# Performance work log

Hardware: AMD Instinct MI355X
Metric: run time of the kernel (lower is better)

The kernel has to match this reference:

```python
import jax, jax.numpy as jnp
import numpy as np

V, B, T, E, H = 16384, 64, 256, 128, 1024


def setup_inputs() -> dict:
    key = jax.random.key(0)
    ks = jax.random.split(key, 10)
    inp = {
        'input_data': jax.random.randint(ks[0], (B, T), 0, V, dtype=jnp.int32),
        'targets': jax.random.randint(ks[1], (B, T), 0, V, dtype=jnp.int32),
        'embedding': jax.random.normal(ks[2], (V, E), dtype=jnp.float32) * 0.02,
        # layer 1 GRU (input E, hidden H): gate kernel [E+H, 2H], candidate kernel [E+H, H]
        'W_g1': jax.random.normal(ks[3], (E + H, 2 * H), dtype=jnp.float32) * 0.05,
        'b_g1': jnp.ones((2 * H,), dtype=jnp.float32),  # TF GRUCell gate bias init = 1.0
        'W_c1': jax.random.normal(ks[4], (E + H, H), dtype=jnp.float32) * 0.05,
        'b_c1': jnp.zeros((H,), dtype=jnp.float32),
        # layer 2 GRU (input H, hidden H)
        'W_g2': jax.random.normal(ks[5], (2 * H, 2 * H), dtype=jnp.float32) * 0.05,
        'b_g2': jnp.ones((2 * H,), dtype=jnp.float32),
        'W_c2': jax.random.normal(ks[6], (2 * H, H), dtype=jnp.float32) * 0.05,
        'b_c2': jnp.zeros((H,), dtype=jnp.float32),
        'softmax_w': jax.random.normal(ks[7], (H, V), dtype=jnp.float32) * 1e-4,
        'softmax_b': jnp.zeros((V,), dtype=jnp.float32),
    }
    return inp


def _gru_step(h, x, W_g, b_g, W_c, b_c):
    # TF GRUCell: r,u = sigmoid([x,h] @ W_g + b_g); c = tanh([x, r*h] @ W_c + b_c)
    ru = jax.nn.sigmoid(jnp.concatenate([x, h], axis=-1) @ W_g + b_g)
    r, u = jnp.split(ru, 2, axis=-1)
    c = jnp.tanh(jnp.concatenate([x, r * h], axis=-1) @ W_c + b_c)
    return u * h + (1.0 - u) * c


def reference(input_data, targets, embedding, W_g1, b_g1, W_c1, b_c1,
              W_g2, b_g2, W_c2, b_c2, softmax_w, softmax_b):
    # inference path: is_training=False, so dropout wrappers are identity
    x = embedding[input_data]               # [B, T, E]
    xs = jnp.transpose(x, (1, 0, 2))        # [T, B, E] time-major for scan

    h0 = (jnp.zeros((B, H), x.dtype), jnp.zeros((B, H), x.dtype))

    def step(carry, x_t):
        h1, h2 = carry
        h1 = _gru_step(h1, x_t, W_g1, b_g1, W_c1, b_c1)
        h2 = _gru_step(h2, h1, W_g2, b_g2, W_c2, b_c2)
        return (h1, h2), h2

    _, ys = jax.lax.scan(step, h0, xs)      # ys: [T, B, H]
    out = jnp.transpose(ys, (1, 0, 2)).reshape(-1, H)  # [B*T, H] batch-major flatten

    logits = out @ softmax_w + softmax_b    # [B*T, V]
    logp = jax.nn.log_softmax(logits, axis=-1)
    flat_t = targets.reshape(-1)
    nll = -jnp.take_along_axis(logp, flat_t[:, None], axis=1)[:, 0]
    loss = jnp.mean(nll)
    return logits, loss
```

## Files before the change

kernel.cpp:

```cpp
#include <hip/hip_runtime.h>

typedef __bf16 bf16_t;
typedef __bf16 bf16x8 __attribute__((ext_vector_type(8)));
typedef float f32x4 __attribute__((ext_vector_type(4)));
typedef float f32x2 __attribute__((ext_vector_type(2)));
typedef unsigned u32x4 __attribute__((ext_vector_type(4)));

constexpr int kB = 64, kT = 256, kE = 128, kH = 1024, kV = 16384;
constexpr int kBT = kB * kT;

__device__ __forceinline__ void ld16_sc(const void* p, u32x4& d) {
    asm volatile("global_load_dwordx4 %0, %1, off sc0 sc1" : "=v"(d) : "v"(p));
}
__device__ __forceinline__ void ld8_sc(const void* p, f32x2& d) {
    asm volatile("global_load_dwordx2 %0, %1, off sc0 sc1" : "=v"(d) : "v"(p));
}
__device__ __forceinline__ void ld8_c(const void* p, f32x2& d) {
    asm volatile("global_load_dwordx2 %0, %1, off" : "=v"(d) : "v"(p));
}
__device__ __forceinline__ void st4_sc(void* p, unsigned v) {
    asm volatile("global_store_dword %0, %1, off sc0 sc1" :: "v"(p), "v"(v));
}
__device__ __forceinline__ void st8_sc(void* p, f32x2 v) {
    asm volatile("global_store_dwordx2 %0, %1, off sc0 sc1" :: "v"(p), "v"(v));
}
__device__ __forceinline__ unsigned ld_flag(const unsigned* p) {
    unsigned v;
    asm volatile("global_load_dword %0, %1, off sc0 sc1\n\ts_waitcnt vmcnt(0)"
                 : "=v"(v) : "v"(p) : "memory");
    return v;
}
#define WAITVM(n) asm volatile("s_waitcnt vmcnt(" #n ")" ::: "memory")

#define GL2LDS(gp, lp) __builtin_amdgcn_global_load_lds( \
    (const __attribute__((address_space(1))) void*)(gp), \
    (__attribute__((address_space(3))) void*)(lp), 16, 0, 0)

__device__ __forceinline__ unsigned pack_bf16(float a, float b) {
    union { unsigned u; __bf16 h[2]; } c;
    c.h[0] = (__bf16)a; c.h[1] = (__bf16)b;
    return c.u;
}
__device__ __forceinline__ f32x2 mk2(float a, float b) {
    f32x2 v; v[0] = a; v[1] = b; return v;
}

__global__ void zero_bytes(char* p, size_t n) {
    size_t stride = (size_t)gridDim.x * blockDim.x * 16;
    for (size_t i = ((size_t)blockIdx.x * blockDim.x + threadIdx.x) * 16; i < n; i += stride) {
        uint4 z; z.x = z.y = z.z = z.w = 0;
        *reinterpret_cast<uint4*>(p + i) = z;
    }
}

__global__ void transpose_to_bf16(const float* __restrict__ src, bf16_t* __restrict__ dst,
                                  int R, int C) {
    __shared__ float tile[32][33];
    int c0 = blockIdx.x * 32, r0 = blockIdx.y * 32;
    for (int rr = threadIdx.y; rr < 32; rr += 8)
        tile[rr][threadIdx.x] = src[(size_t)(r0 + rr) * C + c0 + threadIdx.x];
    __syncthreads();
    for (int rr = threadIdx.y; rr < 32; rr += 8)
        dst[(size_t)(c0 + rr) * R + r0 + threadIdx.x] = (bf16_t)tile[threadIdx.x][rr];
}

__global__ __launch_bounds__(256) void embed_gather(const int* __restrict__ ids,
                                                    const float* __restrict__ emb,
                                                    bf16_t* __restrict__ XB) {
    int base = blockIdx.x * 16;
    for (int idx = threadIdx.x; idx < 16 * kE; idx += 256) {
        int r = idx >> 7, k = idx & 127;
        int row = base + r;
        XB[(size_t)row * kE + k] = (bf16_t)emb[(size_t)ids[row] * kE + k];
    }
}

__global__ __launch_bounds__(256) void xpre_gemm(
    const bf16_t* __restrict__ XB, const bf16_t* __restrict__ WT,
    const float* __restrict__ bias, float* __restrict__ Cout, int N) {
    __shared__ __align__(16) char As[128 * 256];
    __shared__ __align__(16) char Bs[128 * 256];
    const int tid = threadIdx.x;
    const int w = tid >> 6, l = tid & 63, lr = l & 15, lk8 = (l >> 4) * 8;
    const int wr = w >> 1, wc = w & 1;
    const size_t row0 = (size_t)blockIdx.y * 128, col0 = (size_t)blockIdx.x * 128;
    for (int c = tid; c < 2048; c += 256) {
        int o = c * 16; int row = o >> 8; int kk = o & 255;
        int dst = (row << 8) + (kk ^ ((row & 7) << 4));
        *reinterpret_cast<bf16x8*>(As + dst) =
            *reinterpret_cast<const bf16x8*>(XB + (row0 + row) * kE + (kk >> 1));
        *reinterpret_cast<bf16x8*>(Bs + dst) =
            *reinterpret_cast<const bf16x8*>(WT + (col0 + row) * kE + (kk >> 1));
    }
    __syncthreads();
    f32x4 acc[4][4] = {};
    #pragma unroll
    for (int ks = 0; ks < 4; ++ks) {
        int kb = (ks * 32 + lk8) * 2;
        bf16x8 af[4], bfv[4];
        #pragma unroll
        for (int mf = 0; mf < 4; ++mf) {
            int r = wr * 64 + mf * 16 + lr;
            af[mf] = *reinterpret_cast<const bf16x8*>(As + (r << 8) + (kb ^ ((r & 7) << 4)));
        }
        #pragma unroll
        for (int nf = 0; nf < 4; ++nf) {
            int r = wc * 64 + nf * 16 + lr;
            bfv[nf] = *reinterpret_cast<const bf16x8*>(Bs + (r << 8) + (kb ^ ((r & 7) << 4)));
        }
        #pragma unroll
        for (int mf = 0; mf < 4; ++mf)
            #pragma unroll
            for (int nf = 0; nf < 4; ++nf)
                acc[mf][nf] = __builtin_amdgcn_mfma_f32_16x16x32_bf16(af[mf], bfv[nf], acc[mf][nf], 0, 0, 0);
    }
    #pragma unroll
    for (int mf = 0; mf < 4; ++mf) {
        size_t row = row0 + wr * 64 + mf * 16 + (l >> 4) * 4;
        #pragma unroll
        for (int nf = 0; nf < 4; ++nf) {
            size_t col = col0 + wc * 64 + nf * 16 + lr;
            float bvl = bias[col];
            #pragma unroll
            for (int i = 0; i < 4; ++i)
                Cout[(row + i) * (size_t)N + col] = acc[mf][nf][i] + bvl;
        }
    }
}

struct PP {
    const bf16_t *WG1HT, *WC1HT, *WG2T, *WC2T;
    const float *XG1, *XC1;
    const float *bg2, *bc2;
    float *H1F, *H2F, *U1, *U2;
    bf16_t *X2, *X2C0, *X2C1, *RH1, *YS;
    unsigned *flags;
};

__device__ __forceinline__ void wait_flags(const unsigned* flags, int base, int cnt,
                                           unsigned tgt, int lane) {
    if ((unsigned)lane < (unsigned)cnt) {
        const unsigned* p = flags + (size_t)(base + lane) * 16;
        while (ld_flag(p) < tgt) { }
    }
}

template<int RBSH>
__device__ __forceinline__ void mm_part8(const bf16_t* __restrict__ A, int astr,
                                         const char* __restrict__ wl, int kbase,
                                         int w, int lr, int lk, f32x4 (&acc)[4][2]) {
    const int kbeg = w * 256;
    const bf16_t* base[4];
    #pragma unroll
    for (int mf = 0; mf < 4; ++mf)
        base[mf] = A + (size_t)(mf * 16 + lr) * astr + kbeg + lk;
    u32x4 buf[8][4];
    #pragma unroll
    for (int pi = 0; pi < 8; ++pi)
        #pragma unroll
        for (int mf = 0; mf < 4; ++mf)
            ld16_sc(base[mf] + pi * 32, buf[pi][mf]);
    #pragma unroll
    for (int ki = 0; ki < 8; ++ki) {
        if (ki == 0)      WAITVM(28);
        else if (ki == 1) WAITVM(24);
        else if (ki == 2) WAITVM(20);
        else if (ki == 3) WAITVM(16);
        else if (ki == 4) WAITVM(12);
        else if (ki == 5) WAITVM(8);
        else if (ki == 6) WAITVM(4);
        else              WAITVM(0);
        __builtin_amdgcn_sched_barrier(0);
        #pragma unroll
        for (int nf = 0; nf < 2; ++nf) {
            int rr = nf * 16 + lr;
            int kb = (kbase + kbeg + ki * 32 + lk) * 2;
            bf16x8 wv = *reinterpret_cast<const bf16x8*>(wl + (rr << RBSH) + (kb ^ ((rr & 7) << 4)));
            #pragma unroll
            for (int mf = 0; mf < 4; ++mf)
                acc[mf][nf] = __builtin_amdgcn_mfma_f32_16x16x32_bf16(
                    __builtin_bit_cast(bf16x8, buf[ki][mf]), wv, acc[mf][nf], 0, 0, 0);
        }
    }
}

__global__ __launch_bounds__(256, 1) void rnn_persistent(PP P) {
    __shared__ __align__(16) char wlds[131072];
    __shared__ float red[4][64][8];
    const int blk = blockIdx.x, tid = threadIdx.x;
    const int w = tid >> 6, l = tid & 63, lr = l & 15, lk = (l >> 4) * 8;
    int grp, idx;
    if (blk < 64)       { grp = 0; idx = blk; }
    else if (blk < 96)  { grp = 1; idx = blk - 64; }
    else if (blk < 160) { grp = 2; idx = blk - 96; }
    else                { grp = 3; idx = blk - 160; }
    const int n0 = idx * 32;
    const int K = (grp < 2) ? 1024 : 2048;
    const int rbsh = (grp < 2) ? 11 : 12;
    const bf16_t* Wsrc = (grp == 0) ? P.WG1HT : (grp == 1) ? P.WC1HT : (grp == 2) ? P.WG2T : P.WC2T;

    for (int c = tid; c < (32 * K * 2) / 16; c += 256) {
        int o = c * 16;
        int row = o >> rbsh;
        int kk = o & ((1 << rbsh) - 1);
        bf16x8 v = *reinterpret_cast<const bf16x8*>(Wsrc + (size_t)(n0 + row) * K + (kk >> 1));
        *reinterpret_cast<bf16x8*>(wlds + (row << rbsh) + (kk ^ ((row & 7) << 4))) = v;
    }
    __syncthreads();

    const unsigned* F = P.flags;
    const int r = tid >> 2, cb = (tid & 3) * 2;
    const bool lowhalf = (n0 < 1024);

    f32x2 bx[4], hreg[4];
    #pragma unroll
    for (int p = 0; p < 4; ++p) {
        hreg[p] = mk2(0.f, 0.f);
        int j = n0 + p * 8 + cb;
        if (grp == 2)      bx[p] = *reinterpret_cast<const f32x2*>(P.bg2 + j);
        else if (grp == 3) bx[p] = *reinterpret_cast<const f32x2*>(P.bc2 + j);
    }

    for (int t = 0; t < kT; ++t) {
        unsigned ut = (unsigned)t;
        bf16_t* x2c = (t & 1) ? P.X2C1 : P.X2C0;
        f32x4 acc[4][2] = {};
        f32x2 pa[4], px[4];

        if (grp == 0) {
            if (t) wait_flags(F, 64, 32, ut, tid);
            __syncthreads();
            #pragma unroll
            for (int p = 0; p < 4; ++p) {
                int j = n0 + p * 8 + cb;
                ld8_c(P.XG1 + ((size_t)r * kT + t) * 2048 + j, px[p]);
                if (lowhalf) ld8_sc(P.H1F + r * 1024 + j, pa[p]);
            }
            mm_part8<11>(P.X2, 2048, wlds, 0, w, lr, lk, acc);
        } else if (grp == 1) {
            wait_flags(F, 0, 64, ut + 1, tid);
            __syncthreads();
            #pragma unroll
            for (int p = 0; p < 4; ++p) {
                int j = n0 + p * 8 + cb;
                ld8_c(P.XC1 + ((size_t)r * kT + t) * 1024 + j, px[p]);
                ld8_sc(P.U1 + r * 1024 + j, pa[p]);
            }
            mm_part8<11>(P.RH1, 1024, wlds, 0, w, lr, lk, acc);
            if (t) wait_flags(F, 96, 64, ut, tid);
            if (t >= 2) wait_flags(F, 160, 32, ut - 1, tid - 64);
            __syncthreads();
        } else if (grp == 2) {
            if (t) wait_flags(F, 160, 32, ut, tid);
            __syncthreads();
            #pragma unroll
            for (int p = 0; p < 4; ++p) {
                int j = n0 + p * 8 + cb;
                px[p] = bx[p];
                if (lowhalf) ld8_sc(P.H2F + r * 1024 + j, pa[p]);
            }
            mm_part8<12>(P.X2 + 1024, 2048, wlds, 1024, w, lr, lk, acc);
            wait_flags(F, 64, 32, ut + 1, tid);
            __syncthreads();
            mm_part8<12>(P.X2, 2048, wlds, 0, w, lr, lk, acc);
        } else {
            wait_flags(F, 64, 32, ut + 1, tid);
            __syncthreads();
            mm_part8<12>(x2c, 2048, wlds, 0, w, lr, lk, acc);
            wait_flags(F, 96, 64, ut + 1, tid);
            __syncthreads();
            #pragma unroll
            for (int p = 0; p < 4; ++p) {
                int j = n0 + p * 8 + cb;
                px[p] = bx[p];
                ld8_sc(P.U2 + r * 1024 + j, pa[p]);
            }
            mm_part8<12>(x2c + 1024, 2048, wlds, 1024, w, lr, lk, acc);
        }

        __builtin_amdgcn_sched_barrier(0);

        #pragma unroll
        for (int p = 0; p < 4; ++p) {
            const int nf = p >> 1;
            if (((l >> 3) & 1) == (p & 1)) {
                #pragma unroll
                for (int mf = 0; mf < 4; ++mf)
                    #pragma unroll
                    for (int i = 0; i < 4; ++i)
                        red[w][mf * 16 + (l >> 4) * 4 + i][l & 7] = acc[mf][nf][i];
            }
            __syncthreads();
            {
                float v0 = red[0][r][cb] + red[1][r][cb] + red[2][r][cb] + red[3][r][cb];
                float v1 = red[0][r][cb + 1] + red[1][r][cb + 1] + red[2][r][cb + 1] + red[3][r][cb + 1];
                int j = n0 + p * 8 + cb;
                v0 += px[p][0]; v1 += px[p][1];
                if (grp == 0) {
                    float g0 = 1.f / (1.f + __expf(-v0));
                    float g1 = 1.f / (1.f + __expf(-v1));
                    if (lowhalf) {
                        st4_sc(P.RH1 + r * 1024 + j, pack_bf16(g0 * pa[p][0], g1 * pa[p][1]));
                    } else {
                        st8_sc(P.U1 + r * 1024 + j - 1024, mk2(g0, g1));
                    }
                } else if (grp == 1) {
                    float cc0 = tanhf(v0), cc1 = tanhf(v1);
                    float hn0 = pa[p][0] * hreg[p][0] + (1.f - pa[p][0]) * cc0;
                    float hn1 = pa[p][1] * hreg[p][1] + (1.f - pa[p][1]) * cc1;
                    hreg[p] = mk2(hn0, hn1);
                    st8_sc(P.H1F + r * 1024 + j, hreg[p]);
                    unsigned pk = pack_bf16(hn0, hn1);
                    st4_sc(P.X2 + r * 2048 + j, pk);
                    st4_sc(x2c + r * 2048 + j, pk);
                } else if (grp == 2) {
                    float g0 = 1.f / (1.f + __expf(-v0));
                    float g1 = 1.f / (1.f + __expf(-v1));
                    if (lowhalf) {
                        st4_sc(x2c + r * 2048 + 1024 + j, pack_bf16(g0 * pa[p][0], g1 * pa[p][1]));
                    } else {
                        st8_sc(P.U2 + r * 1024 + j - 1024, mk2(g0, g1));
                    }
                } else {
                    float cc0 = tanhf(v0), cc1 = tanhf(v1);
                    float hn0 = pa[p][0] * hreg[p][0] + (1.f - pa[p][0]) * cc0;
                    float hn1 = pa[p][1] * hreg[p][1] + (1.f - pa[p][1]) * cc1;
                    hreg[p] = mk2(hn0, hn1);
                    st8_sc(P.H2F + r * 1024 + j, hreg[p]);
                    unsigned pk = pack_bf16(hn0, hn1);
                    st4_sc(P.X2 + r * 2048 + 1024 + j, pk);
                    *reinterpret_cast<unsigned*>(P.YS + ((size_t)r * kT + t) * 1024 + j) = pk;
                }
            }
            __syncthreads();
        }

        asm volatile("s_waitcnt vmcnt(0)" ::: "memory");
        __syncthreads();
        if (tid == 0)
            st4_sc((void*)&F[(size_t)blk * 16], ut + 1);
    }
}

__global__ __launch_bounds__(256) void logits_gemm(
    const bf16_t* __restrict__ Amat,
    const bf16_t* __restrict__ Bt,
    const float* __restrict__ bias,
    float* __restrict__ out) {
    __shared__ __align__(16) bf16_t As[2][128 * 64];
    __shared__ __align__(16) bf16_t Bs[2][128 * 64];
    const int tid = threadIdx.x;
    const int w = tid >> 6, l = tid & 63;
    const int wr = w >> 1, wc = w & 1;
    const int lr = l & 15, lk8 = (l >> 4) * 8;
    const int row0 = blockIdx.y * 128, col0 = blockIdx.x * 128;

    int srow[4], scol[4];
    #pragma unroll
    for (int v = 0; v < 4; ++v) {
        int idx = v * 256 + tid;
        srow[v] = idx >> 3;
        scol[v] = (idx & 7) * 8;
    }

    f32x4 acc[4][4] = {};
    #pragma unroll
    for (int v = 0; v < 4; ++v) {
        GL2LDS(Amat + (size_t)(row0 + srow[v]) * kH + scol[v], As[0] + srow[v] * 64 + scol[v]);
        GL2LDS(Bt + (size_t)(col0 + srow[v]) * kH + scol[v], Bs[0] + srow[v] * 64 + scol[v]);
    }
    int cur = 0;
    for (int kt = 0; kt < 16; ++kt) {
        if (kt < 15) {
            int ko = (kt + 1) * 64;
            #pragma unroll
            for (int v = 0; v < 4; ++v) {
                GL2LDS(Amat + (size_t)(row0 + srow[v]) * kH + ko + scol[v], As[cur ^ 1] + srow[v] * 64 + scol[v]);
                GL2LDS(Bt + (size_t)(col0 + srow[v]) * kH + ko + scol[v], Bs[cur ^ 1] + srow[v] * 64 + scol[v]);
            }
            WAITVM(8);
        } else {
            WAITVM(0);
        }
        __syncthreads();
        #pragma unroll
        for (int ks = 0; ks < 2; ++ks) {
            bf16x8 af[4], bfv[4];
            #pragma unroll
            for (int mf = 0; mf < 4; ++mf)
                af[mf] = *reinterpret_cast<const bf16x8*>(As[cur] + (wr * 64 + mf * 16 + lr) * 64 + ks * 32 + lk8);
            #pragma unroll
            for (int nf = 0; nf < 4; ++nf)
                bfv[nf] = *reinterpret_cast<const bf16x8*>(Bs[cur] + (wc * 64 + nf * 16 + lr) * 64 + ks * 32 + lk8);
            #pragma unroll
            for (int mf = 0; mf < 4; ++mf)
                #pragma unroll
                for (int nf = 0; nf < 4; ++nf)
                    acc[mf][nf] = __builtin_amdgcn_mfma_f32_16x16x32_bf16(af[mf], bfv[nf], acc[mf][nf], 0, 0, 0);
        }
        __syncthreads();
        cur ^= 1;
    }
    #pragma unroll
    for (int mf = 0; mf < 4; ++mf) {
        int row = row0 + wr * 64 + mf * 16 + (l >> 4) * 4;
        #pragma unroll
        for (int nf = 0; nf < 4; ++nf) {
            int col = col0 + wc * 64 + nf * 16 + lr;
            float bvl = bias[col];
            #pragma unroll
            for (int i = 0; i < 4; ++i)
                out[(size_t)(row + i) * kV + col] = acc[mf][nf][i] + bvl;
        }
    }
}

__global__ __launch_bounds__(256) void row_nll(const float* __restrict__ logits,
                                               const int* __restrict__ targets,
                                               float* __restrict__ nll) {
    int row = blockIdx.x;
    const float* rowp = logits + (size_t)row * kV;
    int tid = threadIdx.x;
    float m = -1e30f, s = 0.f;
    for (int j = tid; j < kV; j += 256) {
        float v = rowp[j];
        if (v > m) { s = s * __expf(m - v) + 1.f; m = v; }
        else s += __expf(v - m);
    }
    __shared__ float ms[256], ss[256];
    ms[tid] = m; ss[tid] = s;
    __syncthreads();
    for (int off = 128; off; off >>= 1) {
        if (tid < off) {
            float m2 = ms[tid + off], s2 = ss[tid + off];
            float M = fmaxf(ms[tid], m2);
            ss[tid] = ss[tid] * __expf(ms[tid] - M) + s2 * __expf(m2 - M);
            ms[tid] = M;
        }
        __syncthreads();
    }
    if (tid == 0) {
        float lse = ms[0] + __logf(ss[0]);
        nll[row] = lse - rowp[targets[row]];
    }
}

__global__ __launch_bounds__(256) void loss_reduce(const float* __restrict__ nll,
                                                   float* __restrict__ out) {
    __shared__ float sm[256];
    int tid = threadIdx.x;
    float s = 0.f;
    for (int i = tid; i < kBT; i += 256) s += nll[i];
    sm[tid] = s;
    __syncthreads();
    for (int off = 128; off; off >>= 1) {
        if (tid < off) sm[tid] += sm[tid + off];
        __syncthreads();
    }
    if (tid == 0) out[0] = sm[0] / (float)kBT;
}

extern "C" void kernel_launch(void* const* d_in, const int* in_sizes, int n_in,
                              void* d_out, int out_size, void* d_ws, size_t ws_size,
                              hipStream_t stream) {
    const int*   ids = (const int*)d_in[0];
    const int*   tgt = (const int*)d_in[1];
    const float* emb = (const float*)d_in[2];
    const float* Wg1 = (const float*)d_in[3];
    const float* bg1 = (const float*)d_in[4];
    const float* Wc1 = (const float*)d_in[5];
    const float* bc1 = (const float*)d_in[6];
    const float* Wg2 = (const float*)d_in[7];
    const float* bg2 = (const float*)d_in[8];
    const float* Wc2 = (const float*)d_in[9];
    const float* bc2 = (const float*)d_in[10];
    const float* sw  = (const float*)d_in[11];
    const float* sb  = (const float*)d_in[12];
    float* out = (float*)d_out;

    char* ws = (char*)d_ws;
    size_t off = 0;
    auto alloc = [&](size_t bytes) -> void* {
        void* p = ws + off;
        off += (bytes + 255) & ~(size_t)255;
        return p;
    };
    bf16_t* WG1HT = (bf16_t*)alloc((size_t)2048 * 1024 * 2);
    bf16_t* WC1HT = (bf16_t*)alloc((size_t)1024 * 1024 * 2);
    bf16_t* WG2T  = (bf16_t*)alloc((size_t)2048 * 2048 * 2);
    bf16_t* WC2T  = (bf16_t*)alloc((size_t)1024 * 2048 * 2);
    bf16_t* SWT   = (bf16_t*)alloc((size_t)kV * kH * 2);
    bf16_t* WG1XT = (bf16_t*)alloc((size_t)2048 * kE * 2);
    bf16_t* WC1XT = (bf16_t*)alloc((size_t)1024 * kE * 2);
    bf16_t* XB    = (bf16_t*)alloc((size_t)kBT * kE * 2);
    float*  XG1   = (float*)alloc((size_t)kBT * 2048 * 4);
    float*  XC1   = (float*)alloc((size_t)kBT * 1024 * 4);
    bf16_t* YS    = (bf16_t*)alloc((size_t)kBT * kH * 2);
    float*  NLL   = (float*)alloc((size_t)kBT * 4);
    char*   zbase = ws + off;
    float*  H1F   = (float*)alloc((size_t)kB * kH * 4);
    float*  H2F   = (float*)alloc((size_t)kB * kH * 4);
    float*  U1    = (float*)alloc((size_t)kB * kH * 4);
    float*  U2    = (float*)alloc((size_t)kB * kH * 4);
    bf16_t* X2    = (bf16_t*)alloc((size_t)kB * 2048 * 2);
    bf16_t* X2C0  = (bf16_t*)alloc((size_t)kB * 2048 * 2);
    bf16_t* X2C1  = (bf16_t*)alloc((size_t)kB * 2048 * 2);
    bf16_t* RH1   = (bf16_t*)alloc((size_t)kB * kH * 2);
    unsigned* FLAGS = (unsigned*)alloc(192 * 16 * 4);
    size_t zlen = (ws + off) - zbase;

    transpose_to_bf16<<<dim3(64, 32), dim3(32, 8), 0, stream>>>(Wg1 + (size_t)kE * 2048, WG1HT, 1024, 2048);
    transpose_to_bf16<<<dim3(32, 32), dim3(32, 8), 0, stream>>>(Wc1 + (size_t)kE * 1024, WC1HT, 1024, 1024);
    transpose_to_bf16<<<dim3(64, 64), dim3(32, 8), 0, stream>>>(Wg2, WG2T, 2048, 2048);
    transpose_to_bf16<<<dim3(32, 64), dim3(32, 8), 0, stream>>>(Wc2, WC2T, 2048, 1024);
    transpose_to_bf16<<<dim3(512, 32), dim3(32, 8), 0, stream>>>(sw, SWT, 1024, 16384);
    transpose_to_bf16<<<dim3(64, 4), dim3(32, 8), 0, stream>>>(Wg1, WG1XT, 128, 2048);
    transpose_to_bf16<<<dim3(32, 4), dim3(32, 8), 0, stream>>>(Wc1, WC1XT, 128, 1024);

    embed_gather<<<kBT / 16, 256, 0, stream>>>(ids, emb, XB);
    xpre_gemm<<<dim3(16, kBT / 128), 256, 0, stream>>>(XB, WG1XT, bg1, XG1, 2048);
    xpre_gemm<<<dim3(8, kBT / 128), 256, 0, stream>>>(XB, WC1XT, bc1, XC1, 1024);
    zero_bytes<<<256, 256, 0, stream>>>(zbase, zlen);

    PP prm;
    prm.WG1HT = WG1HT; prm.WC1HT = WC1HT; prm.WG2T = WG2T; prm.WC2T = WC2T;
    prm.XG1 = XG1; prm.XC1 = XC1; prm.bg2 = bg2; prm.bc2 = bc2;
    prm.H1F = H1F; prm.H2F = H2F; prm.U1 = U1; prm.U2 = U2;
    prm.X2 = X2; prm.X2C0 = X2C0; prm.X2C1 = X2C1; prm.RH1 = RH1; prm.YS = YS;
    prm.flags = FLAGS;
    void* args[] = { &prm };
    hipLaunchCooperativeKernel((const void*)rnn_persistent, dim3(192), dim3(256), args, 0, stream);

    logits_gemm<<<dim3(kV / 128, kBT / 128), 256, 0, stream>>>(YS, SWT, sb, out);
    row_nll<<<kBT, 256, 0, stream>>>(out, tgt, NLL);
    loss_reduce<<<1, 256, 0, stream>>>(NLL, out + (size_t)kBT * kV);
}
```

Baseline: 6.613 ms.

## Cut reduction barriers in persistent GRU epilogue, add spin sleep, swizzle logits tiles

The per-step cross-wave reduction epilogue now stages all accumulator columns into a padded shared buffer at once, using one barrier for layer-1 groups and two half passes for layer-2 groups, instead of four barrier-separated passes. The shared weight buffer and reduction scratch are merged into one dynamically partitioned allocation so the larger scratch fits. The flag spin loop gains s_sleep to reduce memory polling pressure, at the cost of slightly later wakeup. The logits GEMM remaps block indices to group tiles across XCDs for better L2 reuse.

```diff
diff --git a/kernel.cpp b/kernel.cpp
--- a/kernel.cpp
+++ b/kernel.cpp
@@ -141,7 +141,8 @@
                                            unsigned tgt, int lane) {
     if ((unsigned)lane < (unsigned)cnt) {
         const unsigned* p = flags + (size_t)(base + lane) * 16;
-        while (ld_flag(p) < tgt) { }
+        while (ld_flag(p) < tgt)
+            __builtin_amdgcn_s_sleep(1);
     }
 }
 
@@ -185,8 +186,7 @@
 }
 
 __global__ __launch_bounds__(256, 1) void rnn_persistent(PP P) {
-    __shared__ __align__(16) char wlds[131072];
-    __shared__ float red[4][64][8];
+    __shared__ __align__(16) char smem[148480];
     const int blk = blockIdx.x, tid = threadIdx.x;
     const int w = tid >> 6, l = tid & 63, lr = l & 15, lk = (l >> 4) * 8;
     int grp, idx;
@@ -197,6 +197,8 @@
     const int n0 = idx * 32;
     const int K = (grp < 2) ? 1024 : 2048;
     const int rbsh = (grp < 2) ? 11 : 12;
+    char* wlds = smem;
+    float* red = reinterpret_cast<float*>(smem + (size_t)32 * K * 2);
     const bf16_t* Wsrc = (grp == 0) ? P.WG1HT : (grp == 1) ? P.WC1HT : (grp == 2) ? P.WG2T : P.WC2T;
 
     for (int c = tid; c < (32 * K * 2) / 16; c += 256) {
@@ -277,23 +279,24 @@
             }
             mm_part8<12>(x2c + 1024, 2048, wlds, 1024, w, lr, lk, acc);
         }
-
         __builtin_amdgcn_sched_barrier(0);
 
-        #pragma unroll
-        for (int p = 0; p < 4; ++p) {
-            const int nf = p >> 1;
-            if (((l >> 3) & 1) == (p & 1)) {
+        if (grp < 2) {
+            #pragma unroll
+            for (int mf = 0; mf < 4; ++mf)
                 #pragma unroll
-                for (int mf = 0; mf < 4; ++mf)
+                for (int nf = 0; nf < 2; ++nf)
                     #pragma unroll
                     for (int i = 0; i < 4; ++i)
-                        red[w][mf * 16 + (l >> 4) * 4 + i][l & 7] = acc[mf][nf][i];
-            }
-            __syncthreads();
-            {
-                float v0 = red[0][r][cb] + red[1][r][cb] + red[2][r][cb] + red[3][r][cb];
-                float v1 = red[0][r][cb + 1] + red[1][r][cb + 1] + red[2][r][cb + 1] + red[3][r][cb + 1];
+                        red[((w * 64) + mf * 16 + (l >> 4) * 4 + i) * 33 + nf * 16 + (l & 15)] = acc[mf][nf][i];
+            __syncthreads();
+            #pragma unroll
+            for (int p = 0; p < 4; ++p) {
+                int cl = p * 8 + cb;
+                float v0 = red[(0 * 64 + r) * 33 + cl] + red[(1 * 64 + r) * 33 + cl]
+                         + red[(2 * 64 + r) * 33 + cl] + red[(3 * 64 + r) * 33 + cl];
+                float v1 = red[(0 * 64 + r) * 33 + cl + 1] + red[(1 * 64 + r) * 33 + cl + 1]
+                         + red[(2 * 64 + r) * 33 + cl + 1] + red[(3 * 64 + r) * 33 + cl + 1];
                 int j = n0 + p * 8 + cb;
                 v0 += px[p][0]; v1 += px[p][1];
                 if (grp == 0) {
@@ -304,7 +307,7 @@
                     } else {
                         st8_sc(P.U1 + r * 1024 + j - 1024, mk2(g0, g1));
                     }
-                } else if (grp == 1) {
+                } else {
                     float cc0 = tanhf(v0), cc1 = tanhf(v1);
                     float hn0 = pa[p][0] * hreg[p][0] + (1.f - pa[p][0]) * cc0;
                     float hn1 = pa[p][1] * hreg[p][1] + (1.f - pa[p][1]) * cc1;
@@ -313,26 +316,48 @@
                     unsigned pk = pack_bf16(hn0, hn1);
                     st4_sc(P.X2 + r * 2048 + j, pk);
                     st4_sc(x2c + r * 2048 + j, pk);
-                } else if (grp == 2) {
-                    float g0 = 1.f / (1.f + __expf(-v0));
-                    float g1 = 1.f / (1.f + __expf(-v1));
-                    if (lowhalf) {
-                        st4_sc(x2c + r * 2048 + 1024 + j, pack_bf16(g0 * pa[p][0], g1 * pa[p][1]));
+                }
+            }
+        } else {
+            #pragma unroll
+            for (int half = 0; half < 2; ++half) {
+                if (half) __syncthreads();
+                #pragma unroll
+                for (int mf = 0; mf < 4; ++mf)
+                    #pragma unroll
+                    for (int i = 0; i < 4; ++i)
+                        red[((w * 64) + mf * 16 + (l >> 4) * 4 + i) * 17 + (l & 15)] = acc[mf][half][i];
+                __syncthreads();
+                #pragma unroll
+                for (int p2 = 0; p2 < 2; ++p2) {
+                    int p = half * 2 + p2;
+                    int cl = p2 * 8 + cb;
+                    float v0 = red[(0 * 64 + r) * 17 + cl] + red[(1 * 64 + r) * 17 + cl]
+                             + red[(2 * 64 + r) * 17 + cl] + red[(3 * 64 + r) * 17 + cl];
+                    float v1 = red[(0 * 64 + r) * 17 + cl + 1] + red[(1 * 64 + r) * 17 + cl + 1]
+                             + red[(2 * 64 + r) * 17 + cl + 1] + red[(3 * 64 + r) * 17 + cl + 1];
+                    int j = n0 + p * 8 + cb;
+                    v0 += px[p][0]; v1 += px[p][1];
+                    if (grp == 2) {
+                        float g0 = 1.f / (1.f + __expf(-v0));
+                        float g1 = 1.f / (1.f + __expf(-v1));
+                        if (lowhalf) {
+                            st4_sc(x2c + r * 2048 + 1024 + j, pack_bf16(g0 * pa[p][0], g1 * pa[p][1]));
+                        } else {
+                            st8_sc(P.U2 + r * 1024 + j - 1024, mk2(g0, g1));
+                        }
                     } else {
-                        st8_sc(P.U2 + r * 1024 + j - 1024, mk2(g0, g1));
+                        float cc0 = tanhf(v0), cc1 = tanhf(v1);
+                        float hn0 = pa[p][0] * hreg[p][0] + (1.f - pa[p][0]) * cc0;
+                        float hn1 = pa[p][1] * hreg[p][1] + (1.f - pa[p][1]) * cc1;
+                        hreg[p] = mk2(hn0, hn1);
+                        st8_sc(P.H2F + r * 1024 + j, hreg[p]);
+                        unsigned pk = pack_bf16(hn0, hn1);
+                        st4_sc(P.X2 + r * 2048 + 1024 + j, pk);
+                        *reinterpret_cast<unsigned*>(P.YS + ((size_t)r * kT + t) * 1024 + j) = pk;
                     }
-                } else {
-                    float cc0 = tanhf(v0), cc1 = tanhf(v1);
-                    float hn0 = pa[p][0] * hreg[p][0] + (1.f - pa[p][0]) * cc0;
-                    float hn1 = pa[p][1] * hreg[p][1] + (1.f - pa[p][1]) * cc1;
-                    hreg[p] = mk2(hn0, hn1);
-                    st8_sc(P.H2F + r * 1024 + j, hreg[p]);
-                    unsigned pk = pack_bf16(hn0, hn1);
-                    st4_sc(P.X2 + r * 2048 + 1024 + j, pk);
-                    *reinterpret_cast<unsigned*>(P.YS + ((size_t)r * kT + t) * 1024 + j) = pk;
                 }
             }
-            __syncthreads();
         }
 
         asm volatile("s_waitcnt vmcnt(0)" ::: "memory");
@@ -353,7 +378,9 @@
     const int w = tid >> 6, l = tid & 63;
     const int wr = w >> 1, wc = w & 1;
     const int lr = l & 15, lk8 = (l >> 4) * 8;
-    const int row0 = blockIdx.y * 128, col0 = blockIdx.x * 128;
+    int lin = blockIdx.y * gridDim.x + blockIdx.x;
+    int s = (lin & 7) * 2048 + (lin >> 3);
+    const int row0 = (s >> 7) * 128, col0 = (s & 127) * 128;
 
     int srow[4], scol[4];
     #pragma unroll
```

Result: no change. 6.635 ms (+0.3%).
